# Kernel tuning notes

Hardware: AMD Instinct MI355X
Metric: run time of the kernel (lower is better)

Reference implementation:

```python
import jax, jax.numpy as jnp
import numpy as np

B, L, D, F, E = 64, 512, 512, 2048, 8
EPS = 1e-9

def setup_inputs() -> dict:
    key = jax.random.key(0)
    ks = jax.random.split(key, 8)
    x = jax.random.normal(ks[0], (B, L, D), dtype=jnp.float32)
    logits = jax.random.normal(ks[1], (B, E), dtype=jnp.float32)
    moe_masks = jax.random.randint(ks[2], (B, E), 0, 2, dtype=jnp.int32)
    # per-expert MLP params: Linear(D->F), GELU, Linear(F->D)
    w1 = jax.random.normal(ks[3], (E, D, F), dtype=jnp.float32) / np.sqrt(D)
    b1 = jnp.zeros((E, F), dtype=jnp.float32)
    w2 = jax.random.normal(ks[4], (E, F, D), dtype=jnp.float32) / np.sqrt(F)
    b2 = jnp.zeros((E, D), dtype=jnp.float32)
    return {"cycle_curve_data": x, "logits": logits, "moe_masks": moe_masks,
            "w1": w1, "b1": b1, "w2": w2, "b2": b2}

def reference(cycle_curve_data, logits, moe_masks, w1, b1, w2, b2):
    x = cycle_curve_data
    mask = (moe_masks == 1).astype(logits.dtype)           # [B,E]
    raw = jax.nn.softmax(logits, axis=1)                   # [B,E]
    gated = raw * mask
    gates = gated / (jnp.sum(gated, axis=1, keepdims=True) + EPS)  # renormalized [B,E]
    # dispatch/combine: combine == sum_e gates[:,e] * expert_e(x); zero-gate rows
    # contribute nothing, matching the index-based dispatcher exactly.
    out = jnp.zeros_like(x)
    n_exp = w1.shape[0]
    for e in range(n_exp):
        h = jax.nn.gelu(jnp.einsum('bld,df->blf', x, w1[e]) + b1[e], approximate=False)
        y = jnp.einsum('blf,fd->bld', h, w2[e]) + b2[e]
        out = out + gates[:, e, None, None] * y
    bsz = x.shape[0]
    guide_loss = (1.0 - jnp.sum(raw * mask) / bsz) ** 2
    return out, guide_loss
```

## Files before the change

### kernel.cpp

```cpp
#include <hip/hip_runtime.h>
#include <math.h>

#define Bb 64
#define Ll 512
#define Dd 512
#define Ff 2048
#define Ee 8

typedef _Float16 half_t;
typedef _Float16 half8 __attribute__((ext_vector_type(8)));
typedef float f32x4 __attribute__((ext_vector_type(4)));

#define W2T_OFF ((size_t)Ee * Dd * Ff)

__device__ __forceinline__ void dma16(const half_t* g, half_t* l) {
    __builtin_amdgcn_global_load_lds((const __attribute__((address_space(1))) void*)g,
                                     (__attribute__((address_space(3))) void*)l, 16, 0, 0);
}
__device__ __forceinline__ void dma16f(const float* g, float* l) {
    __builtin_amdgcn_global_load_lds((const __attribute__((address_space(1))) void*)g,
                                     (__attribute__((address_space(3))) void*)l, 16, 0, 0);
}

#define VWAIT(n)  asm volatile("s_waitcnt vmcnt(" #n ")" ::: "memory")
#define VLWAIT(n) asm volatile("s_waitcnt vmcnt(" #n ") lgkmcnt(0)" ::: "memory")
#define BAR() do { __builtin_amdgcn_s_barrier();                 \
                   asm volatile("" ::: "memory");                \
                   __builtin_amdgcn_sched_barrier(0); } while (0)

__global__ __launch_bounds__(256)
void prep_transpose(const float* __restrict__ w1, const float* __restrict__ w2,
                    half_t* __restrict__ ws)
{
    __shared__ half_t T[64 * 72];
    int bid = blockIdx.x;
    const float* src; half_t* dst; int R, C, r0, c0;
    if (bid < 2048) {
        int e = bid >> 8, t = bid & 255;
        r0 = (t >> 5) * 64; c0 = (t & 31) * 64;
        src = w1 + (size_t)e * Dd * Ff;
        dst = ws + (size_t)e * Ff * Dd;
        R = Dd; C = Ff;
    } else {
        bid -= 2048;
        int e = bid >> 8, t = bid & 255;
        r0 = (t >> 3) * 64; c0 = (t & 7) * 64;
        src = w2 + (size_t)e * Ff * Dd;
        dst = ws + W2T_OFF + (size_t)e * Dd * Ff;
        R = Ff; C = Dd;
    }
    const int cx = threadIdx.x & 63, ry = threadIdx.x >> 6;
    #pragma unroll
    for (int j = 0; j < 16; ++j) {
        int r = ry * 16 + j;
        T[cx * 72 + r] = (half_t)src[(size_t)(r0 + r) * C + c0 + cx];
    }
    __syncthreads();
    const int rx = threadIdx.x & 7;
    #pragma unroll
    for (int it = 0; it < 2; ++it) {
        int cr = (threadIdx.x >> 3) + it * 32;
        *(half8*)&dst[(size_t)(c0 + cr) * R + r0 + rx * 8] = *(half8*)&T[cr * 72 + rx * 8];
    }
}

__global__ __launch_bounds__(512, 2)
void moe_main(const float* __restrict__ x, const float* __restrict__ logits,
              const int* __restrict__ masks, const half_t* __restrict__ ws,
              const float* __restrict__ b1, const float* __restrict__ b2,
              float* __restrict__ out)
{
    __shared__ half_t Wbuf[3][128 * 128];
    __shared__ half_t Hs[64 * 128];
    __shared__ float  Bs[128];

    const int tid  = threadIdx.x;
    const int wv   = tid >> 6;
    const int lane = tid & 63;
    const int nl   = lane & 15;
    const int q    = lane >> 4;
    const int mt   = wv >> 1;
    const int nh   = wv & 1;
    const int rl   = lane >> 4;
    const int pcl  = lane & 15;

    const int bid = blockIdx.x;

    int b;
    {
        int cj = 0;
        #pragma unroll
        for (int e2 = 0; e2 < Ee; ++e2) cj += (masks[lane * Ee + e2] == 1);
        int rj = 0;
        for (int k = 0; k < Bb; ++k) {
            const int ck = __shfl(cj, k);
            rj += (ck > cj) || (ck == cj && k < lane);
        }
        const unsigned long long mword = __ballot(rj == (bid >> 3));
        b = (int)__builtin_ctzll(mword);
    }
    const int l0 = (bid & 7) * 64;

    float mx = -1e30f;
    #pragma unroll
    for (int e = 0; e < Ee; ++e) mx = fmaxf(mx, logits[b * Ee + e]);
    float s = 0.f, gs = 0.f;
    unsigned am = 0u;
    #pragma unroll
    for (int e = 0; e < Ee; ++e) {
        const float ex = expf(logits[b * Ee + e] - mx);
        s += ex;
        if (masks[b * Ee + e] == 1) { gs += ex; am |= (1u << e); }
    }
    const int el = lane & 7;
    const float myg = ((am >> el) & 1u)
        ? expf(logits[b * Ee + el] - mx) / (gs + 1e-9f * s) : 0.f;
    float ge[Ee];
    #pragma unroll
    for (int e = 0; e < Ee; ++e) ge[e] = __shfl(myg, e);

    half8 afrag[16];
    {
        const float* xrow = x + (size_t)(b * Ll + l0 + mt * 16 + nl) * Dd;
        #pragma unroll
        for (int ks = 0; ks < 16; ++ks) {
            const int c0 = ks * 32 + q * 8;
            const f32x4 u0 = *(const f32x4*)(xrow + c0);
            const f32x4 u1 = *(const f32x4*)(xrow + c0 + 4);
            half8 a;
            a[0]=(half_t)u0[0]; a[1]=(half_t)u0[1]; a[2]=(half_t)u0[2]; a[3]=(half_t)u0[3];
            a[4]=(half_t)u1[0]; a[5]=(half_t)u1[1]; a[6]=(half_t)u1[2]; a[7]=(half_t)u1[3];
            afrag[ks] = a;
        }
    }

    f32x4 oacc[16];
    #pragma unroll
    for (int i = 0; i < 16; ++i) oacc[i] = (f32x4){0.f, 0.f, 0.f, 0.f};

    auto stageT = [&](const half_t* src, int ld, half_t* dst) {
        #pragma unroll
        for (int ss = 0; ss < 4; ++ss) {
            const int row = wv * 16 + ss * 4 + rl;
            const int c = pcl ^ (row & 15);
            dma16(src + (size_t)row * ld + c * 8, dst + (wv * 16 + ss * 4) * 128);
        }
    };
    auto computeA = [&](const half8* af, const half_t* Wb, f32x4* hc) {
        #pragma unroll
        for (int ks = 0; ks < 4; ++ks) {
            const half8 a = af[ks];
            #pragma unroll
            for (int nf = 0; nf < 4; ++nf) {
                const int row = nh * 64 + nf * 16 + nl;
                const half8 bf = *(const half8*)&Wb[row * 128 + (((ks * 4 + q) ^ nl) * 8)];
                hc[nf] = __builtin_amdgcn_mfma_f32_16x16x32_f16(a, bf, hc[nf], 0, 0, 0);
            }
        }
    };
    auto computeB = [&](const half8* ha, const half_t* Wb, f32x4* oc) {
        #pragma unroll
        for (int ks = 0; ks < 4; ++ks) {
            #pragma unroll
            for (int t = 0; t < 4; ++t) {
                const int lr = t * 32 + nh * 16 + nl;
                const half8 bf = *(const half8*)&Wb[lr * 128 + (((ks * 4 + q) ^ nl) * 8)];
                oc[t] = __builtin_amdgcn_mfma_f32_16x16x32_f16(ha[ks], bf, oc[t], 0, 0, 0);
            }
        }
    };

    int cur = 0;
    unsigned rem = am;
    if (rem) {
        const int e0 = (int)__builtin_ctz(rem);
        const half_t* W1p = ws + (size_t)e0 * Ff * Dd;
        asm volatile("s_waitcnt vmcnt(0)" ::: "memory");
        stageT(W1p,       Dd, Wbuf[0]);
        if (lane < 32) dma16f(b1 + (size_t)e0 * Ff + lane * 4, Bs);
        stageT(W1p + 128, Dd, Wbuf[1]);
        VWAIT(4);
        BAR();
    }

    while (rem) {
        const int e = (int)__builtin_ctz(rem); rem &= rem - 1u;
        const int en = rem ? (int)__builtin_ctz(rem) : -1;
        const float g = __shfl(myg, e);
        const half_t* W1te = ws + (size_t)e * Ff * Dd;
        const half_t* W2te = ws + W2T_OFF + (size_t)e * Dd * Ff;
        const half_t* W1nx = (en >= 0) ? ws + (size_t)en * Ff * Dd : W1te;
        const float*  b1nx = (en >= 0) ? b1 + (size_t)en * Ff : b1;

        #pragma unroll 1
        for (int fci = 0; fci < 16; ++fci) {
            const int f0 = fci * 128;
            const half_t* WA = W1te + (size_t)f0 * Dd;
            const half_t* WB = W2te + f0;
            const bool hn = (fci < 15) || (en >= 0);
            const half_t* An = (fci < 15) ? (WA + (size_t)128 * Dd) : W1nx;
            const float*  bn = (fci < 15) ? (b1 + (size_t)e * Ff + f0 + 128) : b1nx;

            f32x4 hacc[4];
            #pragma unroll
            for (int i = 0; i < 4; ++i) hacc[i] = (f32x4){0.f, 0.f, 0.f, 0.f};

            { half_t* Wp = Wbuf[cur ? cur - 1 : 2];
              stageT(WA + 2 * 128, Dd, Wp);
              computeA(&afrag[0], Wbuf[cur], hacc);
              VWAIT(4); BAR(); cur = (cur == 2) ? 0 : cur + 1; }
            { half_t* Wp = Wbuf[cur ? cur - 1 : 2];
              stageT(WA + 3 * 128, Dd, Wp);
              computeA(&afrag[4], Wbuf[cur], hacc);
              VWAIT(4); BAR(); cur = (cur == 2) ? 0 : cur + 1; }
            { half_t* Wp = Wbuf[cur ? cur - 1 : 2];
              stageT(WB, Ff, Wp);
              computeA(&afrag[8], Wbuf[cur], hacc);
              VWAIT(4); BAR(); cur = (cur == 2) ? 0 : cur + 1; }
            { half_t* Wp = Wbuf[cur ? cur - 1 : 2];
              stageT(WB + (size_t)128 * Ff, Ff, Wp);
              computeA(&afrag[12], Wbuf[cur], hacc);
              #pragma unroll
              for (int nf = 0; nf < 4; ++nf) {
                  const int fl = nh * 64 + nf * 16 + nl;
                  const float bv = Bs[fl];
                  #pragma unroll
                  for (int r = 0; r < 4; ++r) {
                      const int m = mt * 16 + q * 4 + r;
                      const float v  = hacc[nf][r] + bv;
                      const float gl = 0.5f * v * (1.f + erff(v * 0.70710678118654752f));
                      const int blk = (fl >> 3) ^ (m & 15);
                      Hs[m * 128 + blk * 8 + (fl & 7)] = (half_t)(g * gl);
                  }
              }
              VLWAIT(4); BAR(); cur = (cur == 2) ? 0 : cur + 1; }

            half8 ha[4];
            { half_t* Wp = Wbuf[cur ? cur - 1 : 2];
              #pragma unroll
              for (int ks = 0; ks < 4; ++ks)
                  ha[ks] = *(const half8*)&Hs[(mt * 16 + nl) * 128 + (((ks * 4 + q) ^ nl) * 8)];
              stageT(WB + (size_t)256 * Ff, Ff, Wp);
              computeB(ha, Wbuf[cur], &oacc[0]);
              VWAIT(4); BAR(); cur = (cur == 2) ? 0 : cur + 1; }
            { half_t* Wp = Wbuf[cur ? cur - 1 : 2];
              stageT(WB + (size_t)384 * Ff, Ff, Wp);
              computeB(ha, Wbuf[cur], &oacc[4]);
              VWAIT(4); BAR(); cur = (cur == 2) ? 0 : cur + 1; }
            { half_t* Wp = Wbuf[cur ? cur - 1 : 2];
              if (hn) {
                  stageT(An, Dd, Wp);
                  if (lane < 32) dma16f(bn + lane * 4, Bs);
              }
              computeB(ha, Wbuf[cur], &oacc[8]);
              if (hn) { VWAIT(5); } else { VWAIT(0); }
              BAR(); cur = (cur == 2) ? 0 : cur + 1; }
            { half_t* Wp = Wbuf[cur ? cur - 1 : 2];
              if (hn) stageT(An + 128, Dd, Wp);
              computeB(ha, Wbuf[cur], &oacc[12]);
              if (hn) { VWAIT(4); } else { VWAIT(0); }
              BAR(); cur = (cur == 2) ? 0 : cur + 1; }
        }
    }

    #pragma unroll
    for (int ncc = 0; ncc < 4; ++ncc) {
        #pragma unroll
        for (int t = 0; t < 4; ++t) {
            const int dcol = ncc * 128 + t * 32 + nh * 16 + nl;
            float bb = 0.f;
            #pragma unroll
            for (int e = 0; e < Ee; ++e) bb += ge[e] * b2[e * Dd + dcol];
            const f32x4 v = oacc[ncc * 4 + t];
            const size_t base = (size_t)(b * Ll + l0 + mt * 16 + q * 4) * Dd + dcol;
            out[base]          = v[0] + bb;
            out[base + Dd]     = v[1] + bb;
            out[base + 2 * Dd] = v[2] + bb;
            out[base + 3 * Dd] = v[3] + bb;
        }
    }
}

__global__ void moe_loss(const float* __restrict__ logits, const int* __restrict__ masks,
                         float* __restrict__ loss_out)
{
    const int b = threadIdx.x;
    float lg[Ee];
    float mx = -1e30f;
    #pragma unroll
    for (int e = 0; e < Ee; ++e) { lg[e] = logits[b * Ee + e]; mx = fmaxf(mx, lg[e]); }
    float s = 0.f;
    #pragma unroll
    for (int e = 0; e < Ee; ++e) { float ex = expf(lg[e] - mx); s += ex; lg[e] = ex; }
    float rs = 0.f;
    #pragma unroll
    for (int e = 0; e < Ee; ++e) if (masks[b * Ee + e] == 1) rs += lg[e] / s;
    #pragma unroll
    for (int off = 32; off > 0; off >>= 1) rs += __shfl_down(rs, off);
    if (b == 0) {
        const float t = 1.f - rs / (float)Bb;
        loss_out[0] = t * t;
    }
}

extern "C" void kernel_launch(void* const* d_in, const int* in_sizes, int n_in,
                              void* d_out, int out_size, void* d_ws, size_t ws_size,
                              hipStream_t stream)
{
    const float* x      = (const float*)d_in[0];
    const float* logits = (const float*)d_in[1];
    const int*   masks  = (const int*)d_in[2];
    const float* w1     = (const float*)d_in[3];
    const float* b1     = (const float*)d_in[4];
    const float* w2     = (const float*)d_in[5];
    const float* b2     = (const float*)d_in[6];
    float* out = (float*)d_out;
    half_t* ws = (half_t*)d_ws;

    hipLaunchKernelGGL(prep_transpose, dim3(4096), dim3(256), 0, stream, w1, w2, ws);
    hipLaunchKernelGGL(moe_main, dim3(512), dim3(512), 0, stream,
                       x, logits, masks, ws, b1, b2, out);
    hipLaunchKernelGGL(moe_loss, dim3(1), dim3(64), 0, stream,
                       logits, masks, out + (size_t)Bb * Ll * Dd);
}
```

Measured before the change: 1.623 ms.

## Deepen weight staging pipeline to four LDS buffers and reorder block-to-batch mapping

Grows the LDS weight ring buffer from three to four 128x128 tiles so each step prefetches two tiles ahead instead of one, with the vmcnt waits and staging offsets adjusted to match. The goal is to hide more global-load latency behind the MFMA work. It also changes how block IDs map to batch rank and sequence chunk, so concurrently running blocks fall on different batches. The extra 32KB of LDS per block may cut occupancy below the two blocks per CU requested by the launch bounds.

```diff
diff --git a/kernel.cpp b/kernel.cpp
--- a/kernel.cpp
+++ b/kernel.cpp
@@ -70,7 +70,7 @@
               const float* __restrict__ b1, const float* __restrict__ b2,
               float* __restrict__ out)
 {
-    __shared__ half_t Wbuf[3][128 * 128];
+    __shared__ half_t Wbuf[4][128 * 128];
     __shared__ half_t Hs[64 * 128];
     __shared__ float  Bs[128];
 
@@ -85,6 +85,8 @@
     const int pcl  = lane & 15;
 
     const int bid = blockIdx.x;
+    const int rk = (bid >> 6) * 8 + (bid & 7);
+    const int l0 = ((bid >> 3) & 7) * 64;
 
     int b;
     {
@@ -96,10 +98,9 @@
             const int ck = __shfl(cj, k);
             rj += (ck > cj) || (ck == cj && k < lane);
         }
-        const unsigned long long mword = __ballot(rj == (bid >> 3));
+        const unsigned long long mword = __ballot(rj == rk);
         b = (int)__builtin_ctzll(mword);
     }
-    const int l0 = (bid & 7) * 64;
 
     float mx = -1e30f;
     #pragma unroll
@@ -179,7 +180,8 @@
         stageT(W1p,       Dd, Wbuf[0]);
         if (lane < 32) dma16f(b1 + (size_t)e0 * Ff + lane * 4, Bs);
         stageT(W1p + 128, Dd, Wbuf[1]);
-        VWAIT(4);
+        stageT(W1p + 256, Dd, Wbuf[2]);
+        VWAIT(9);
         BAR();
     }
 
@@ -205,20 +207,20 @@
             #pragma unroll
             for (int i = 0; i < 4; ++i) hacc[i] = (f32x4){0.f, 0.f, 0.f, 0.f};
 
-            { half_t* Wp = Wbuf[cur ? cur - 1 : 2];
-              stageT(WA + 2 * 128, Dd, Wp);
+            { half_t* Wp = Wbuf[(cur + 3) & 3];
+              stageT(WA + 3 * 128, Dd, Wp);
               computeA(&afrag[0], Wbuf[cur], hacc);
-              VWAIT(4); BAR(); cur = (cur == 2) ? 0 : cur + 1; }
-            { half_t* Wp = Wbuf[cur ? cur - 1 : 2];
-              stageT(WA + 3 * 128, Dd, Wp);
+              VWAIT(8); BAR(); cur = (cur + 1) & 3; }
+            { half_t* Wp = Wbuf[(cur + 3) & 3];
+              stageT(WB, Ff, Wp);
               computeA(&afrag[4], Wbuf[cur], hacc);
-              VWAIT(4); BAR(); cur = (cur == 2) ? 0 : cur + 1; }
-            { half_t* Wp = Wbuf[cur ? cur - 1 : 2];
-              stageT(WB, Ff, Wp);
+              VWAIT(8); BAR(); cur = (cur + 1) & 3; }
+            { half_t* Wp = Wbuf[(cur + 3) & 3];
+              stageT(WB + (size_t)128 * Ff, Ff, Wp);
               computeA(&afrag[8], Wbuf[cur], hacc);
-              VWAIT(4); BAR(); cur = (cur == 2) ? 0 : cur + 1; }
-            { half_t* Wp = Wbuf[cur ? cur - 1 : 2];
-              stageT(WB + (size_t)128 * Ff, Ff, Wp);
+              VWAIT(8); BAR(); cur = (cur + 1) & 3; }
+            { half_t* Wp = Wbuf[(cur + 3) & 3];
+              stageT(WB + (size_t)256 * Ff, Ff, Wp);
               computeA(&afrag[12], Wbuf[cur], hacc);
               #pragma unroll
               for (int nf = 0; nf < 4; ++nf) {
@@ -233,33 +235,34 @@
                       Hs[m * 128 + blk * 8 + (fl & 7)] = (half_t)(g * gl);
                   }
               }
-              VLWAIT(4); BAR(); cur = (cur == 2) ? 0 : cur + 1; }
+              VLWAIT(8); BAR(); cur = (cur + 1) & 3; }
 
             half8 ha[4];
-            { half_t* Wp = Wbuf[cur ? cur - 1 : 2];
+            { half_t* Wp = Wbuf[(cur + 3) & 3];
               #pragma unroll
               for (int ks = 0; ks < 4; ++ks)
                   ha[ks] = *(const half8*)&Hs[(mt * 16 + nl) * 128 + (((ks * 4 + q) ^ nl) * 8)];
-              stageT(WB + (size_t)256 * Ff, Ff, Wp);
+              stageT(WB + (size_t)384 * Ff, Ff, Wp);
               computeB(ha, Wbuf[cur], &oacc[0]);
-              VWAIT(4); BAR(); cur = (cur == 2) ? 0 : cur + 1; }
-            { half_t* Wp = Wbuf[cur ? cur - 1 : 2];
-              stageT(WB + (size_t)384 * Ff, Ff, Wp);
-              computeB(ha, Wbuf[cur], &oacc[4]);
-              VWAIT(4); BAR(); cur = (cur == 2) ? 0 : cur + 1; }
-            { half_t* Wp = Wbuf[cur ? cur - 1 : 2];
+              VWAIT(8); BAR(); cur = (cur + 1) & 3; }
+            { half_t* Wp = Wbuf[(cur + 3) & 3];
               if (hn) {
                   stageT(An, Dd, Wp);
                   if (lane < 32) dma16f(bn + lane * 4, Bs);
               }
+              computeB(ha, Wbuf[cur], &oacc[4]);
+              if (hn) { VWAIT(9); } else { VWAIT(4); }
+              BAR(); cur = (cur + 1) & 3; }
+            { half_t* Wp = Wbuf[(cur + 3) & 3];
+              if (hn) stageT(An + 128, Dd, Wp);
               computeB(ha, Wbuf[cur], &oacc[8]);
-              if (hn) { VWAIT(5); } else { VWAIT(0); }
-              BAR(); cur = (cur == 2) ? 0 : cur + 1; }
-            { half_t* Wp = Wbuf[cur ? cur - 1 : 2];
-              if (hn) stageT(An + 128, Dd, Wp);
+              if (hn) { VWAIT(9); } else { VWAIT(0); }
+              BAR(); cur = (cur + 1) & 3; }
+            { half_t* Wp = Wbuf[(cur + 3) & 3];
+              if (hn) stageT(An + 256, Dd, Wp);
               computeB(ha, Wbuf[cur], &oacc[12]);
-              if (hn) { VWAIT(4); } else { VWAIT(0); }
-              BAR(); cur = (cur == 2) ? 0 : cur + 1; }
+              if (hn) { VWAIT(9); } else { VWAIT(0); }
+              BAR(); cur = (cur + 1) & 3; }
         }
     }
 
```

Result: slower. 2.203 ms (+35.7%).

## Halve per-block row tile to 32 and simplify to double-buffered weight staging

Applied to the files above, without the earlier changes.

Shrinks each workgroup from 512 to 256 threads covering 32 sequence rows instead of 64, doubling the grid to 1024 blocks. Weight staging drops from a three-buffer ring with hand-placed vmcnt waits to two buffers synchronised by __syncthreads. The first-layer bias is now read straight from global memory rather than DMA'd into LDS, and cross-expert prefetch of the next expert's first weight chunk is dropped. The aim is more resident blocks and simpler control flow. The cost is that each weight tile is now reused over half as many rows, so weight traffic roughly doubles and load latency is less hidden.

```diff
diff --git a/kernel.cpp b/kernel.cpp
--- a/kernel.cpp
+++ b/kernel.cpp
@@ -17,16 +17,6 @@
     __builtin_amdgcn_global_load_lds((const __attribute__((address_space(1))) void*)g,
                                      (__attribute__((address_space(3))) void*)l, 16, 0, 0);
 }
-__device__ __forceinline__ void dma16f(const float* g, float* l) {
-    __builtin_amdgcn_global_load_lds((const __attribute__((address_space(1))) void*)g,
-                                     (__attribute__((address_space(3))) void*)l, 16, 0, 0);
-}
-
-#define VWAIT(n)  asm volatile("s_waitcnt vmcnt(" #n ")" ::: "memory")
-#define VLWAIT(n) asm volatile("s_waitcnt vmcnt(" #n ") lgkmcnt(0)" ::: "memory")
-#define BAR() do { __builtin_amdgcn_s_barrier();                 \
-                   asm volatile("" ::: "memory");                \
-                   __builtin_amdgcn_sched_barrier(0); } while (0)
 
 __global__ __launch_bounds__(256)
 void prep_transpose(const float* __restrict__ w1, const float* __restrict__ w2,
@@ -64,15 +54,14 @@
     }
 }
 
-__global__ __launch_bounds__(512, 2)
+__global__ __launch_bounds__(256, 2)
 void moe_main(const float* __restrict__ x, const float* __restrict__ logits,
               const int* __restrict__ masks, const half_t* __restrict__ ws,
               const float* __restrict__ b1, const float* __restrict__ b2,
               float* __restrict__ out)
 {
-    __shared__ half_t Wbuf[3][128 * 128];
-    __shared__ half_t Hs[64 * 128];
-    __shared__ float  Bs[128];
+    __shared__ half_t Wbuf[2][128 * 128];
+    __shared__ half_t Hs[32 * 128];
 
     const int tid  = threadIdx.x;
     const int wv   = tid >> 6;
@@ -85,6 +74,8 @@
     const int pcl  = lane & 15;
 
     const int bid = blockIdx.x;
+    const int rk  = bid >> 4;
+    const int l0  = (bid & 15) * 32;
 
     int b;
     {
@@ -96,10 +87,9 @@
             const int ck = __shfl(cj, k);
             rj += (ck > cj) || (ck == cj && k < lane);
         }
-        const unsigned long long mword = __ballot(rj == (bid >> 3));
+        const unsigned long long mword = __ballot(rj == rk);
         b = (int)__builtin_ctzll(mword);
     }
-    const int l0 = (bid & 7) * 64;
 
     float mx = -1e30f;
     #pragma unroll
@@ -140,10 +130,10 @@
 
     auto stageT = [&](const half_t* src, int ld, half_t* dst) {
         #pragma unroll
-        for (int ss = 0; ss < 4; ++ss) {
-            const int row = wv * 16 + ss * 4 + rl;
+        for (int ss = 0; ss < 8; ++ss) {
+            const int row = wv * 32 + ss * 4 + rl;
             const int c = pcl ^ (row & 15);
-            dma16(src + (size_t)row * ld + c * 8, dst + (wv * 16 + ss * 4) * 128);
+            dma16(src + (size_t)row * ld + c * 8, dst + (wv * 32 + ss * 4) * 128);
         }
     };
     auto computeA = [&](const half8* af, const half_t* Wb, f32x4* hc) {
@@ -170,96 +160,68 @@
         }
     };
 
-    int cur = 0;
     unsigned rem = am;
-    if (rem) {
-        const int e0 = (int)__builtin_ctz(rem);
-        const half_t* W1p = ws + (size_t)e0 * Ff * Dd;
-        asm volatile("s_waitcnt vmcnt(0)" ::: "memory");
-        stageT(W1p,       Dd, Wbuf[0]);
-        if (lane < 32) dma16f(b1 + (size_t)e0 * Ff + lane * 4, Bs);
-        stageT(W1p + 128, Dd, Wbuf[1]);
-        VWAIT(4);
-        BAR();
-    }
-
+    #pragma unroll 1
     while (rem) {
         const int e = (int)__builtin_ctz(rem); rem &= rem - 1u;
-        const int en = rem ? (int)__builtin_ctz(rem) : -1;
         const float g = __shfl(myg, e);
         const half_t* W1te = ws + (size_t)e * Ff * Dd;
         const half_t* W2te = ws + W2T_OFF + (size_t)e * Dd * Ff;
-        const half_t* W1nx = (en >= 0) ? ws + (size_t)en * Ff * Dd : W1te;
-        const float*  b1nx = (en >= 0) ? b1 + (size_t)en * Ff : b1;
+        const float*  b1e  = b1 + (size_t)e * Ff;
+
+        stageT(W1te, Dd, Wbuf[0]);
 
         #pragma unroll 1
         for (int fci = 0; fci < 16; ++fci) {
             const int f0 = fci * 128;
             const half_t* WA = W1te + (size_t)f0 * Dd;
             const half_t* WB = W2te + f0;
-            const bool hn = (fci < 15) || (en >= 0);
-            const half_t* An = (fci < 15) ? (WA + (size_t)128 * Dd) : W1nx;
-            const float*  bn = (fci < 15) ? (b1 + (size_t)e * Ff + f0 + 128) : b1nx;
 
             f32x4 hacc[4];
             #pragma unroll
             for (int i = 0; i < 4; ++i) hacc[i] = (f32x4){0.f, 0.f, 0.f, 0.f};
 
-            { half_t* Wp = Wbuf[cur ? cur - 1 : 2];
-              stageT(WA + 2 * 128, Dd, Wp);
-              computeA(&afrag[0], Wbuf[cur], hacc);
-              VWAIT(4); BAR(); cur = (cur == 2) ? 0 : cur + 1; }
-            { half_t* Wp = Wbuf[cur ? cur - 1 : 2];
-              stageT(WA + 3 * 128, Dd, Wp);
-              computeA(&afrag[4], Wbuf[cur], hacc);
-              VWAIT(4); BAR(); cur = (cur == 2) ? 0 : cur + 1; }
-            { half_t* Wp = Wbuf[cur ? cur - 1 : 2];
-              stageT(WB, Ff, Wp);
-              computeA(&afrag[8], Wbuf[cur], hacc);
-              VWAIT(4); BAR(); cur = (cur == 2) ? 0 : cur + 1; }
-            { half_t* Wp = Wbuf[cur ? cur - 1 : 2];
-              stageT(WB + (size_t)128 * Ff, Ff, Wp);
-              computeA(&afrag[12], Wbuf[cur], hacc);
-              #pragma unroll
-              for (int nf = 0; nf < 4; ++nf) {
-                  const int fl = nh * 64 + nf * 16 + nl;
-                  const float bv = Bs[fl];
-                  #pragma unroll
-                  for (int r = 0; r < 4; ++r) {
-                      const int m = mt * 16 + q * 4 + r;
-                      const float v  = hacc[nf][r] + bv;
-                      const float gl = 0.5f * v * (1.f + erff(v * 0.70710678118654752f));
-                      const int blk = (fl >> 3) ^ (m & 15);
-                      Hs[m * 128 + blk * 8 + (fl & 7)] = (half_t)(g * gl);
-                  }
-              }
-              VLWAIT(4); BAR(); cur = (cur == 2) ? 0 : cur + 1; }
+            #pragma unroll
+            for (int kc = 0; kc < 4; ++kc) {
+                __syncthreads();
+                if (kc < 3) {
+                    stageT(WA + (kc + 1) * 128, Dd, Wbuf[(kc & 1) ^ 1]);
+                } else {
+                    stageT(WB, Ff, Wbuf[(kc & 1) ^ 1]);
+                }
+                computeA(&afrag[kc * 4], Wbuf[kc & 1], hacc);
+            }
+
+            #pragma unroll
+            for (int nf = 0; nf < 4; ++nf) {
+                const int fl = nh * 64 + nf * 16 + nl;
+                const float bv = b1e[f0 + fl];
+                #pragma unroll
+                for (int r = 0; r < 4; ++r) {
+                    const int m = mt * 16 + q * 4 + r;
+                    const float v  = hacc[nf][r] + bv;
+                    const float gl = 0.5f * v * (1.f + erff(v * 0.70710678118654752f));
+                    const int blk = (fl >> 3) ^ (m & 15);
+                    Hs[m * 128 + blk * 8 + (fl & 7)] = (half_t)(g * gl);
+                }
+            }
 
             half8 ha[4];
-            { half_t* Wp = Wbuf[cur ? cur - 1 : 2];
-              #pragma unroll
-              for (int ks = 0; ks < 4; ++ks)
-                  ha[ks] = *(const half8*)&Hs[(mt * 16 + nl) * 128 + (((ks * 4 + q) ^ nl) * 8)];
-              stageT(WB + (size_t)256 * Ff, Ff, Wp);
-              computeB(ha, Wbuf[cur], &oacc[0]);
-              VWAIT(4); BAR(); cur = (cur == 2) ? 0 : cur + 1; }
-            { half_t* Wp = Wbuf[cur ? cur - 1 : 2];
-              stageT(WB + (size_t)384 * Ff, Ff, Wp);
-              computeB(ha, Wbuf[cur], &oacc[4]);
-              VWAIT(4); BAR(); cur = (cur == 2) ? 0 : cur + 1; }
-            { half_t* Wp = Wbuf[cur ? cur - 1 : 2];
-              if (hn) {
-                  stageT(An, Dd, Wp);
-                  if (lane < 32) dma16f(bn + lane * 4, Bs);
-              }
-              computeB(ha, Wbuf[cur], &oacc[8]);
-              if (hn) { VWAIT(5); } else { VWAIT(0); }
-              BAR(); cur = (cur == 2) ? 0 : cur + 1; }
-            { half_t* Wp = Wbuf[cur ? cur - 1 : 2];
-              if (hn) stageT(An + 128, Dd, Wp);
-              computeB(ha, Wbuf[cur], &oacc[12]);
-              if (hn) { VWAIT(4); } else { VWAIT(0); }
-              BAR(); cur = (cur == 2) ? 0 : cur + 1; }
+            #pragma unroll
+            for (int nc = 0; nc < 4; ++nc) {
+                __syncthreads();
+                if (nc == 0) {
+                    #pragma unroll
+                    for (int ks = 0; ks < 4; ++ks)
+                        ha[ks] = *(const half8*)&Hs[(mt * 16 + nl) * 128 + (((ks * 4 + q) ^ nl) * 8)];
+                }
+                if (nc < 3) {
+                    stageT(WB + (size_t)(nc + 1) * 128 * Ff, Ff, Wbuf[(nc & 1) ^ 1]);
+                } else if (fci < 15) {
+                    stageT(WA + (size_t)128 * Dd, Dd, Wbuf[(nc & 1) ^ 1]);
+                }
+                computeB(ha, Wbuf[nc & 1], &oacc[nc * 4]);
+            }
         }
     }
 
@@ -318,7 +280,7 @@
     half_t* ws = (half_t*)d_ws;
 
     hipLaunchKernelGGL(prep_transpose, dim3(4096), dim3(256), 0, stream, w1, w2, ws);
-    hipLaunchKernelGGL(moe_main, dim3(512), dim3(512), 0, stream,
+    hipLaunchKernelGGL(moe_main, dim3(1024), dim3(256), 0, stream,
                        x, logits, masks, ws, b1, b2, out);
     hipLaunchKernelGGL(moe_loss, dim3(1), dim3(64), 0, stream,
                        logits, masks, out + (size_t)Bb * Ll * Dd);
```

After: 2.509 ms. 54.6% more time.

## Split MoE work per expert across blocks with atomic output accumulation

Applied to the files above, without the earlier changes.

Before, each block looped over all active experts for one (batch, 64-row) tile, and blocks were sorted by active-expert count. Now the grid is expanded to one block per (expert, batch, tile), and blocks for masked-out experts exit early. Each block accumulates its gated expert output into global memory with atomicAdd, after a new bias_init kernel writes the combined b2 bias. This targets load imbalance and low parallelism (512 blocks), at the cost of float atomics over the output, an extra full write pass, and nondeterministic summation order.

```diff
diff --git a/kernel.cpp b/kernel.cpp
--- a/kernel.cpp
+++ b/kernel.cpp
@@ -10,6 +10,7 @@
 typedef _Float16 half_t;
 typedef _Float16 half8 __attribute__((ext_vector_type(8)));
 typedef float f32x4 __attribute__((ext_vector_type(4)));
+typedef float f32x2 __attribute__((ext_vector_type(2)));
 
 #define W2T_OFF ((size_t)Ee * Dd * Ff)
 
@@ -64,15 +65,54 @@
     }
 }
 
+__global__ __launch_bounds__(256)
+void bias_init(const float* __restrict__ logits, const int* __restrict__ masks,
+               const float* __restrict__ b2, float* __restrict__ out)
+{
+    const int b  = blockIdx.x >> 3;
+    const int lc = blockIdx.x & 7;
+    float mx = -1e30f;
+    #pragma unroll
+    for (int e = 0; e < Ee; ++e) mx = fmaxf(mx, logits[b * Ee + e]);
+    float s = 0.f, gs = 0.f;
+    #pragma unroll
+    for (int e = 0; e < Ee; ++e) {
+        const float ex = expf(logits[b * Ee + e] - mx);
+        s += ex;
+        if (masks[b * Ee + e] == 1) gs += ex;
+    }
+    const float inv = 1.f / (gs + 1e-9f * s);
+    const int d0 = threadIdx.x * 2;
+    f32x2 bb = (f32x2){0.f, 0.f};
+    #pragma unroll
+    for (int e = 0; e < Ee; ++e) {
+        const float g = (masks[b * Ee + e] == 1)
+                      ? expf(logits[b * Ee + e] - mx) * inv : 0.f;
+        bb[0] += g * b2[e * Dd + d0];
+        bb[1] += g * b2[e * Dd + d0 + 1];
+    }
+    float* dst = out + (size_t)(b * Ll + lc * 64) * Dd + d0;
+    #pragma unroll 4
+    for (int l = 0; l < 64; ++l)
+        *(f32x2*)(dst + (size_t)l * Dd) = bb;
+}
+
 __global__ __launch_bounds__(512, 2)
 void moe_main(const float* __restrict__ x, const float* __restrict__ logits,
               const int* __restrict__ masks, const half_t* __restrict__ ws,
-              const float* __restrict__ b1, const float* __restrict__ b2,
-              float* __restrict__ out)
+              const float* __restrict__ b1, float* __restrict__ out)
 {
     __shared__ half_t Wbuf[3][128 * 128];
     __shared__ half_t Hs[64 * 128];
     __shared__ float  Bs[128];
+
+    const int bid = blockIdx.x;
+    const int e   = bid >> 9;
+    const int bl  = bid & 511;
+    const int b   = bl >> 3;
+    const int l0  = (bl & 7) * 64;
+
+    if (masks[b * Ee + e] != 1) return;
 
     const int tid  = threadIdx.x;
     const int wv   = tid >> 6;
@@ -84,40 +124,17 @@
     const int rl   = lane >> 4;
     const int pcl  = lane & 15;
 
-    const int bid = blockIdx.x;
-
-    int b;
-    {
-        int cj = 0;
-        #pragma unroll
-        for (int e2 = 0; e2 < Ee; ++e2) cj += (masks[lane * Ee + e2] == 1);
-        int rj = 0;
-        for (int k = 0; k < Bb; ++k) {
-            const int ck = __shfl(cj, k);
-            rj += (ck > cj) || (ck == cj && k < lane);
-        }
-        const unsigned long long mword = __ballot(rj == (bid >> 3));
-        b = (int)__builtin_ctzll(mword);
-    }
-    const int l0 = (bid & 7) * 64;
-
     float mx = -1e30f;
     #pragma unroll
-    for (int e = 0; e < Ee; ++e) mx = fmaxf(mx, logits[b * Ee + e]);
+    for (int e2 = 0; e2 < Ee; ++e2) mx = fmaxf(mx, logits[b * Ee + e2]);
     float s = 0.f, gs = 0.f;
-    unsigned am = 0u;
-    #pragma unroll
-    for (int e = 0; e < Ee; ++e) {
-        const float ex = expf(logits[b * Ee + e] - mx);
+    #pragma unroll
+    for (int e2 = 0; e2 < Ee; ++e2) {
+        const float ex = expf(logits[b * Ee + e2] - mx);
         s += ex;
-        if (masks[b * Ee + e] == 1) { gs += ex; am |= (1u << e); }
-    }
-    const int el = lane & 7;
-    const float myg = ((am >> el) & 1u)
-        ? expf(logits[b * Ee + el] - mx) / (gs + 1e-9f * s) : 0.f;
-    float ge[Ee];
-    #pragma unroll
-    for (int e = 0; e < Ee; ++e) ge[e] = __shfl(myg, e);
+        if (masks[b * Ee + e2] == 1) gs += ex;
+    }
+    const float g = expf(logits[b * Ee + e] - mx) / (gs + 1e-9f * s);
 
     half8 afrag[16];
     {
@@ -170,97 +187,86 @@
         }
     };
 
+    const half_t* W1te = ws + (size_t)e * Ff * Dd;
+    const half_t* W2te = ws + W2T_OFF + (size_t)e * Dd * Ff;
+    const float*  b1e  = b1 + (size_t)e * Ff;
+
     int cur = 0;
-    unsigned rem = am;
-    if (rem) {
-        const int e0 = (int)__builtin_ctz(rem);
-        const half_t* W1p = ws + (size_t)e0 * Ff * Dd;
-        asm volatile("s_waitcnt vmcnt(0)" ::: "memory");
-        stageT(W1p,       Dd, Wbuf[0]);
-        if (lane < 32) dma16f(b1 + (size_t)e0 * Ff + lane * 4, Bs);
-        stageT(W1p + 128, Dd, Wbuf[1]);
-        VWAIT(4);
-        BAR();
-    }
-
-    while (rem) {
-        const int e = (int)__builtin_ctz(rem); rem &= rem - 1u;
-        const int en = rem ? (int)__builtin_ctz(rem) : -1;
-        const float g = __shfl(myg, e);
-        const half_t* W1te = ws + (size_t)e * Ff * Dd;
-        const half_t* W2te = ws + W2T_OFF + (size_t)e * Dd * Ff;
-        const half_t* W1nx = (en >= 0) ? ws + (size_t)en * Ff * Dd : W1te;
-        const float*  b1nx = (en >= 0) ? b1 + (size_t)en * Ff : b1;
-
-        #pragma unroll 1
-        for (int fci = 0; fci < 16; ++fci) {
-            const int f0 = fci * 128;
-            const half_t* WA = W1te + (size_t)f0 * Dd;
-            const half_t* WB = W2te + f0;
-            const bool hn = (fci < 15) || (en >= 0);
-            const half_t* An = (fci < 15) ? (WA + (size_t)128 * Dd) : W1nx;
-            const float*  bn = (fci < 15) ? (b1 + (size_t)e * Ff + f0 + 128) : b1nx;
-
-            f32x4 hacc[4];
-            #pragma unroll
-            for (int i = 0; i < 4; ++i) hacc[i] = (f32x4){0.f, 0.f, 0.f, 0.f};
-
-            { half_t* Wp = Wbuf[cur ? cur - 1 : 2];
-              stageT(WA + 2 * 128, Dd, Wp);
-              computeA(&afrag[0], Wbuf[cur], hacc);
-              VWAIT(4); BAR(); cur = (cur == 2) ? 0 : cur + 1; }
-            { half_t* Wp = Wbuf[cur ? cur - 1 : 2];
-              stageT(WA + 3 * 128, Dd, Wp);
-              computeA(&afrag[4], Wbuf[cur], hacc);
-              VWAIT(4); BAR(); cur = (cur == 2) ? 0 : cur + 1; }
-            { half_t* Wp = Wbuf[cur ? cur - 1 : 2];
-              stageT(WB, Ff, Wp);
-              computeA(&afrag[8], Wbuf[cur], hacc);
-              VWAIT(4); BAR(); cur = (cur == 2) ? 0 : cur + 1; }
-            { half_t* Wp = Wbuf[cur ? cur - 1 : 2];
-              stageT(WB + (size_t)128 * Ff, Ff, Wp);
-              computeA(&afrag[12], Wbuf[cur], hacc);
+    asm volatile("s_waitcnt vmcnt(0)" ::: "memory");
+    stageT(W1te,       Dd, Wbuf[0]);
+    if (lane < 32) dma16f(b1e + lane * 4, Bs);
+    stageT(W1te + 128, Dd, Wbuf[1]);
+    VWAIT(4);
+    BAR();
+
+    #pragma unroll 1
+    for (int fci = 0; fci < 16; ++fci) {
+        const int f0 = fci * 128;
+        const half_t* WA = W1te + (size_t)f0 * Dd;
+        const half_t* WB = W2te + f0;
+        const bool hn = (fci < 15);
+        const half_t* An = WA + (size_t)128 * Dd;
+        const float*  bn = b1e + f0 + 128;
+
+        f32x4 hacc[4];
+        #pragma unroll
+        for (int i = 0; i < 4; ++i) hacc[i] = (f32x4){0.f, 0.f, 0.f, 0.f};
+
+        { half_t* Wp = Wbuf[cur ? cur - 1 : 2];
+          stageT(WA + 2 * 128, Dd, Wp);
+          computeA(&afrag[0], Wbuf[cur], hacc);
+          VWAIT(4); BAR(); cur = (cur == 2) ? 0 : cur + 1; }
+        { half_t* Wp = Wbuf[cur ? cur - 1 : 2];
+          stageT(WA + 3 * 128, Dd, Wp);
+          computeA(&afrag[4], Wbuf[cur], hacc);
+          VWAIT(4); BAR(); cur = (cur == 2) ? 0 : cur + 1; }
+        { half_t* Wp = Wbuf[cur ? cur - 1 : 2];
+          stageT(WB, Ff, Wp);
+          computeA(&afrag[8], Wbuf[cur], hacc);
+          VWAIT(4); BAR(); cur = (cur == 2) ? 0 : cur + 1; }
+        { half_t* Wp = Wbuf[cur ? cur - 1 : 2];
+          stageT(WB + (size_t)128 * Ff, Ff, Wp);
+          computeA(&afrag[12], Wbuf[cur], hacc);
+          #pragma unroll
+          for (int nf = 0; nf < 4; ++nf) {
+              const int fl = nh * 64 + nf * 16 + nl;
+              const float bv = Bs[fl];
               #pragma unroll
-              for (int nf = 0; nf < 4; ++nf) {
-                  const int fl = nh * 64 + nf * 16 + nl;
-                  const float bv = Bs[fl];
-                  #pragma unroll
-                  for (int r = 0; r < 4; ++r) {
-                      const int m = mt * 16 + q * 4 + r;
-                      const float v  = hacc[nf][r] + bv;
-                      const float gl = 0.5f * v * (1.f + erff(v * 0.70710678118654752f));
-                      const int blk = (fl >> 3) ^ (m & 15);
-                      Hs[m * 128 + blk * 8 + (fl & 7)] = (half_t)(g * gl);
-                  }
+              for (int r = 0; r < 4; ++r) {
+                  const int m = mt * 16 + q * 4 + r;
+                  const float v  = hacc[nf][r] + bv;
+                  const float gl = 0.5f * v * (1.f + erff(v * 0.70710678118654752f));
+                  const int blk = (fl >> 3) ^ (m & 15);
+                  Hs[m * 128 + blk * 8 + (fl & 7)] = (half_t)(g * gl);
               }
-              VLWAIT(4); BAR(); cur = (cur == 2) ? 0 : cur + 1; }
-
-            half8 ha[4];
-            { half_t* Wp = Wbuf[cur ? cur - 1 : 2];
-              #pragma unroll
-              for (int ks = 0; ks < 4; ++ks)
-                  ha[ks] = *(const half8*)&Hs[(mt * 16 + nl) * 128 + (((ks * 4 + q) ^ nl) * 8)];
-              stageT(WB + (size_t)256 * Ff, Ff, Wp);
-              computeB(ha, Wbuf[cur], &oacc[0]);
-              VWAIT(4); BAR(); cur = (cur == 2) ? 0 : cur + 1; }
-            { half_t* Wp = Wbuf[cur ? cur - 1 : 2];
-              stageT(WB + (size_t)384 * Ff, Ff, Wp);
-              computeB(ha, Wbuf[cur], &oacc[4]);
-              VWAIT(4); BAR(); cur = (cur == 2) ? 0 : cur + 1; }
-            { half_t* Wp = Wbuf[cur ? cur - 1 : 2];
-              if (hn) {
-                  stageT(An, Dd, Wp);
-                  if (lane < 32) dma16f(bn + lane * 4, Bs);
-              }
-              computeB(ha, Wbuf[cur], &oacc[8]);
-              if (hn) { VWAIT(5); } else { VWAIT(0); }
-              BAR(); cur = (cur == 2) ? 0 : cur + 1; }
-            { half_t* Wp = Wbuf[cur ? cur - 1 : 2];
-              if (hn) stageT(An + 128, Dd, Wp);
-              computeB(ha, Wbuf[cur], &oacc[12]);
-              if (hn) { VWAIT(4); } else { VWAIT(0); }
-              BAR(); cur = (cur == 2) ? 0 : cur + 1; }
-        }
+          }
+          VLWAIT(4); BAR(); cur = (cur == 2) ? 0 : cur + 1; }
+
+        half8 ha[4];
+        { half_t* Wp = Wbuf[cur ? cur - 1 : 2];
+          #pragma unroll
+          for (int ks = 0; ks < 4; ++ks)
+              ha[ks] = *(const half8*)&Hs[(mt * 16 + nl) * 128 + (((ks * 4 + q) ^ nl) * 8)];
+          stageT(WB + (size_t)256 * Ff, Ff, Wp);
+          computeB(ha, Wbuf[cur], &oacc[0]);
+          VWAIT(4); BAR(); cur = (cur == 2) ? 0 : cur + 1; }
+        { half_t* Wp = Wbuf[cur ? cur - 1 : 2];
+          stageT(WB + (size_t)384 * Ff, Ff, Wp);
+          computeB(ha, Wbuf[cur], &oacc[4]);
+          VWAIT(4); BAR(); cur = (cur == 2) ? 0 : cur + 1; }
+        { half_t* Wp = Wbuf[cur ? cur - 1 : 2];
+          if (hn) {
+              stageT(An, Dd, Wp);
+              if (lane < 32) dma16f(bn + lane * 4, Bs);
+          }
+          computeB(ha, Wbuf[cur], &oacc[8]);
+          if (hn) { VWAIT(5); } else { VWAIT(0); }
+          BAR(); cur = (cur == 2) ? 0 : cur + 1; }
+        { half_t* Wp = Wbuf[cur ? cur - 1 : 2];
+          if (hn) stageT(An + 128, Dd, Wp);
+          computeB(ha, Wbuf[cur], &oacc[12]);
+          if (hn) { VWAIT(4); } else { VWAIT(0); }
+          BAR(); cur = (cur == 2) ? 0 : cur + 1; }
     }
 
     #pragma unroll
@@ -268,15 +274,12 @@
         #pragma unroll
         for (int t = 0; t < 4; ++t) {
             const int dcol = ncc * 128 + t * 32 + nh * 16 + nl;
-            float bb = 0.f;
-            #pragma unroll
-            for (int e = 0; e < Ee; ++e) bb += ge[e] * b2[e * Dd + dcol];
             const f32x4 v = oacc[ncc * 4 + t];
-            const size_t base = (size_t)(b * Ll + l0 + mt * 16 + q * 4) * Dd + dcol;
-            out[base]          = v[0] + bb;
-            out[base + Dd]     = v[1] + bb;
-            out[base + 2 * Dd] = v[2] + bb;
-            out[base + 3 * Dd] = v[3] + bb;
+            float* po = out + (size_t)(b * Ll + l0 + mt * 16 + q * 4) * Dd + dcol;
+            atomicAdd(po,          v[0]);
+            atomicAdd(po + Dd,     v[1]);
+            atomicAdd(po + 2 * Dd, v[2]);
+            atomicAdd(po + 3 * Dd, v[3]);
         }
     }
 }
@@ -318,8 +321,9 @@
     half_t* ws = (half_t*)d_ws;
 
     hipLaunchKernelGGL(prep_transpose, dim3(4096), dim3(256), 0, stream, w1, w2, ws);
-    hipLaunchKernelGGL(moe_main, dim3(512), dim3(512), 0, stream,
-                       x, logits, masks, ws, b1, b2, out);
+    hipLaunchKernelGGL(bias_init, dim3(512), dim3(256), 0, stream, logits, masks, b2, out);
+    hipLaunchKernelGGL(moe_main, dim3(4096), dim3(512), 0, stream,
+                       x, logits, masks, ws, b1, out);
     hipLaunchKernelGGL(moe_loss, dim3(1), dim3(64), 0, stream,
                        logits, masks, out + (size_t)Bb * Ll * Dd);
 }
```

Result: slower. 1.923 ms (+18.5%).
